# Kernel tuning notes

Hardware: AMD Instinct MI355X
Metric: run time of the kernel (lower is better)

## Reference

```python
import jax, jax.numpy as jnp
import numpy as np

DIM = 4096
N_HEADS = 32
HEAD_DIM = DIM // N_HEADS  # 128
BSZ = 2
SEQLEN = 2048


def setup_inputs() -> dict:
    key = jax.random.key(0)
    ks = jax.random.split(key, 8)
    x = jax.random.normal(ks[0], (BSZ, SEQLEN, DIM), dtype=jnp.float32)
    # rotary frequencies (LLaMA): theta = 10000^{-2i/d}, angle = pos * theta
    inv_freq = 1.0 / (10000.0 ** (np.arange(0, HEAD_DIM, 2, dtype=np.float32) / HEAD_DIM))
    angles = np.arange(SEQLEN, dtype=np.float32)[:, None] * inv_freq[None, :]  # [S, hd/2]
    freqs_cos = jnp.asarray(np.cos(angles))
    freqs_sin = jnp.asarray(np.sin(angles))
    # causal additive mask [1,1,S,S]
    neg = jnp.float32(-1e9)
    mask = jnp.where(jnp.tril(jnp.ones((SEQLEN, SEQLEN), dtype=bool)), 0.0, neg)[None, None]
    scale = 0.02
    wq = jax.random.normal(ks[1], (DIM, DIM), dtype=jnp.float32) * scale
    wk = jax.random.normal(ks[2], (DIM, DIM), dtype=jnp.float32) * scale
    wv = jax.random.normal(ks[3], (DIM, DIM), dtype=jnp.float32) * scale
    wo = jax.random.normal(ks[4], (DIM, DIM), dtype=jnp.float32) * scale
    return {"x": x, "start_pos": 0, "freqs_cos": freqs_cos, "freqs_sin": freqs_sin,
            "mask": mask, "wq": wq, "wk": wk, "wv": wv, "wo": wo}


def _apply_rotary(t, cos, sin):
    # t: [B,S,H,hd]; cos/sin: [S,hd/2] -> broadcast [1,S,1,hd/2]
    t = t.reshape(*t.shape[:-1], HEAD_DIM // 2, 2)
    t0, t1 = t[..., 0], t[..., 1]
    c = cos[None, :, None, :]
    s = sin[None, :, None, :]
    r0 = t0 * c - t1 * s
    r1 = t0 * s + t1 * c
    return jnp.stack([r0, r1], axis=-1).reshape(*t0.shape[:-1], HEAD_DIM)


def reference(x, start_pos, freqs_cos, freqs_sin, mask, wq, wk, wv, wo):
    bsz, seqlen, _ = x.shape
    # QKV projections (nn.Linear: y = x @ W.T; weights stored [out,in])
    xq = (x @ wq.T).reshape(bsz, seqlen, N_HEADS, HEAD_DIM)
    xk = (x @ wk.T).reshape(bsz, seqlen, N_HEADS, HEAD_DIM)
    xv = (x @ wv.T).reshape(bsz, seqlen, N_HEADS, HEAD_DIM)
    xq = _apply_rotary(xq, freqs_cos, freqs_sin)
    xk = _apply_rotary(xk, freqs_cos, freqs_sin)
    # [B,H,S,hd]
    q = xq.transpose(0, 2, 1, 3)
    k = xk.transpose(0, 2, 1, 3)
    v = xv.transpose(0, 2, 1, 3)
    scale = 1.0 / jnp.sqrt(jnp.float32(HEAD_DIM))
    scores = jnp.einsum('bhqd,bhkd->bhqk', q, k) * scale + mask
    probs = jax.nn.softmax(scores, axis=-1)
    out = jnp.einsum('bhqk,bhkd->bhqd', probs, v)  # [B,H,S,hd]
    out = out.transpose(0, 2, 1, 3).reshape(bsz, seqlen, DIM)
    return out @ wo.T
```

## Files before the change

kernel.cpp:

```cpp
#include <hip/hip_runtime.h>

typedef unsigned short ushort_t;
typedef unsigned int u32;
typedef short bf16x8 __attribute__((ext_vector_type(8)));
typedef float f32x4 __attribute__((ext_vector_type(4)));
typedef float f32x16 __attribute__((ext_vector_type(16)));
typedef u32 u32x4 __attribute__((ext_vector_type(4)));

__device__ __forceinline__ ushort_t f2bf(float f) {
  u32 u = __builtin_bit_cast(u32, f);
  u += 0x7FFFu + ((u >> 16) & 1u);
  return (ushort_t)(u >> 16);
}
__device__ __forceinline__ float bf2f(u32 bits16) {
  return __builtin_bit_cast(float, bits16 << 16);
}

__global__ __launch_bounds__(256)
void cvt_kernel(const float* __restrict__ in, ushort_t* __restrict__ out) {
  const int i = blockIdx.x * 256 + threadIdx.x;
  const float4 a = ((const float4*)in)[(size_t)i * 2];
  const float4 b = ((const float4*)in)[(size_t)i * 2 + 1];
  uint4 r;
  r.x = (u32)f2bf(a.x) | ((u32)f2bf(a.y) << 16);
  r.y = (u32)f2bf(a.z) | ((u32)f2bf(a.w) << 16);
  r.z = (u32)f2bf(b.x) | ((u32)f2bf(b.y) << 16);
  r.w = (u32)f2bf(b.z) | ((u32)f2bf(b.w) << 16);
  ((uint4*)out)[i] = r;
}

template <int F32OUT>
__global__ __launch_bounds__(512, 2)
void gemm256(const ushort_t* __restrict__ A, const ushort_t* __restrict__ B,
             void* __restrict__ C) {
  constexpr int KD = 4096, ND = 4096;
  __shared__ ushort_t sA[2][2][128 * 64];
  __shared__ ushort_t sB[2][2][128 * 64];
  const int tid = threadIdx.x;
  const int lane = tid & 63, wave = tid >> 6;
  const int lq = lane & 15, g = lane >> 4;
  const int wm = wave >> 2, wn = wave & 3;
  const int id = blockIdx.x;
  const int swz = (id & 7) * 32 + (id >> 3);
  const int bm = (swz >> 4) * 256;
  const int bn = (swz & 15) * 256;
  const int csw = ((lane & 7) ^ (lane >> 3)) * 8;
  const int srow = lane >> 3;

  f32x4 acc[8][4];
#pragma unroll
  for (int m = 0; m < 8; ++m)
#pragma unroll
    for (int n = 0; n < 4; ++n) acc[m][n] = (f32x4)0.f;

#define STG(sbuf, G, rowb, t_, s_, h_)                                               \
  {                                                                                  \
    _Pragma("unroll") for (int i_ = 0; i_ < 2; ++i_) {                               \
      const int r0_ = wave * 16 + i_ * 8;                                            \
      const int tc_ = (t_) > 63 ? 63 : (t_);                                         \
      const ushort_t* src_ =                                                         \
          (G) + (size_t)((rowb) + (h_) * 128 + r0_ + srow) * KD + tc_ * 64 + csw;    \
      __builtin_amdgcn_global_load_lds(                                              \
          (const __attribute__((address_space(1))) u32*)src_,                        \
          (__attribute__((address_space(3))) u32*)&sbuf[s_][h_][r0_ * 64 + lane * 8],\
          16, 0, 0);                                                                 \
    }                                                                                \
  }
#define RD_A(S_, H_, mf_, kk_)                                                        \
  (*(const bf16x8*)&sA[S_][H_][(wm * 64 + (mf_) * 16 + lq) * 64 +                     \
                               ((((kk_) * 4 + g) ^ (lq & 7)) * 8)])
#define RD_B(S_, H_, nf_, kk_)                                                        \
  (*(const bf16x8*)&sB[S_][H_][(wn * 32 + (nf_) * 16 + lq) * 64 +                     \
                               ((((kk_) * 4 + g) ^ (lq & 7)) * 8)])
#define MM2(MB, B0R, B1R)                                                             \
  _Pragma("unroll") for (int mf = 0; mf < 4; ++mf)                                    \
    _Pragma("unroll") for (int nf = 0; nf < 2; ++nf)                                  \
      _Pragma("unroll") for (int kk = 0; kk < 2; ++kk) {                              \
        acc[(MB) + mf][nf] = __builtin_amdgcn_mfma_f32_16x16x32_bf16(                 \
            af[mf][kk], B0R[nf][kk], acc[(MB) + mf][nf], 0, 0, 0);                    \
        acc[(MB) + mf][2 + nf] = __builtin_amdgcn_mfma_f32_16x16x32_bf16(             \
            af[mf][kk], B1R[nf][kk], acc[(MB) + mf][2 + nf], 0, 0, 0);                \
      }

  STG(sA, A, bm, 0, 0, 0); STG(sA, A, bm, 0, 0, 1);
  STG(sB, B, bn, 0, 0, 0); STG(sB, B, bn, 0, 0, 1);
  asm volatile("s_waitcnt vmcnt(0)" ::: "memory");
  __builtin_amdgcn_s_barrier();
  __builtin_amdgcn_sched_barrier(0);

  bf16x8 af[4][2], b0[2][2], b1[2][2];

#define TILE(S_, T_)                                                                  \
  STG(sA, A, bm, (T_) + 1, (S_) ^ 1, 0);                                              \
  STG(sA, A, bm, (T_) + 1, (S_) ^ 1, 1);                                              \
  STG(sB, B, bn, (T_) + 1, (S_) ^ 1, 0);                                              \
  STG(sB, B, bn, (T_) + 1, (S_) ^ 1, 1);                                              \
  _Pragma("unroll") for (int mf = 0; mf < 4; ++mf)                                    \
    _Pragma("unroll") for (int kk = 0; kk < 2; ++kk)                                  \
      af[mf][kk] = RD_A(S_, 0, mf, kk);                                               \
  _Pragma("unroll") for (int nf = 0; nf < 2; ++nf)                                    \
    _Pragma("unroll") for (int kk = 0; kk < 2; ++kk) {                                \
      b0[nf][kk] = RD_B(S_, 0, nf, kk);                                               \
      b1[nf][kk] = RD_B(S_, 1, nf, kk);                                               \
    }                                                                                 \
  __builtin_amdgcn_s_setprio(1);                                                      \
  MM2(0, b0, b1);                                                                     \
  __builtin_amdgcn_s_setprio(0);                                                      \
  _Pragma("unroll") for (int mf = 0; mf < 4; ++mf)                                    \
    _Pragma("unroll") for (int kk = 0; kk < 2; ++kk)                                  \
      af[mf][kk] = RD_A(S_, 1, mf, kk);                                               \
  __builtin_amdgcn_s_setprio(1);                                                      \
  MM2(4, b0, b1);                                                                     \
  __builtin_amdgcn_s_setprio(0);                                                      \
  asm volatile("s_waitcnt vmcnt(0)" ::: "memory");                                    \
  __builtin_amdgcn_s_barrier();                                                       \
  __builtin_amdgcn_sched_barrier(0);

  for (int t = 0; t < 64; t += 2) {
    TILE(0, t)
    TILE(1, t + 1)
  }
#undef TILE
#undef STG
#undef RD_A
#undef RD_B
#undef MM2

#pragma unroll
  for (int m = 0; m < 8; ++m) {
    const int grow = bm + (m >> 2) * 128 + wm * 64 + (m & 3) * 16 + g * 4;
#pragma unroll
    for (int r = 0; r < 4; ++r)
#pragma unroll
      for (int n = 0; n < 4; ++n) {
        const int gcol = bn + (n >> 1) * 128 + wn * 32 + (n & 1) * 16 + lq;
        if (F32OUT)
          ((float*)C)[(size_t)(grow + r) * ND + gcol] = acc[m][n][r];
        else
          ((ushort_t*)C)[(size_t)(grow + r) * ND + gcol] = f2bf(acc[m][n][r]);
      }
  }
}

__global__ __launch_bounds__(256)
void rope_kernel(ushort_t* __restrict__ Q, ushort_t* __restrict__ K,
                 const float* __restrict__ fcos, const float* __restrict__ fsin) {
  const int gid = blockIdx.x * 256 + threadIdx.x;
  ushort_t* T = blockIdx.y ? K : Q;
  const float scale = blockIdx.y ? 1.f : 0.08838834764831845f;
  const int j8 = gid & 15;
  const int h = (gid >> 4) & 31;
  const int s = (gid >> 9) & 2047;
  const int b = gid >> 20;
  const size_t off = (size_t)(b * 2048 + s) * 4096 + h * 128 + j8 * 8;
  uint4 v = *(const uint4*)(T + off);
  const float4 c4 = *(const float4*)(fcos + s * 64 + j8 * 4);
  const float4 s4 = *(const float4*)(fsin + s * 64 + j8 * 4);
  u32 w[4] = {v.x, v.y, v.z, v.w};
  const float cc[4] = {c4.x, c4.y, c4.z, c4.w};
  const float ss[4] = {s4.x, s4.y, s4.z, s4.w};
#pragma unroll
  for (int p = 0; p < 4; ++p) {
    const float t0 = bf2f(w[p] & 0xffffu);
    const float t1 = bf2f(w[p] >> 16);
    const float r0 = (t0 * cc[p] - t1 * ss[p]) * scale;
    const float r1 = (t0 * ss[p] + t1 * cc[p]) * scale;
    w[p] = (u32)f2bf(r0) | ((u32)f2bf(r1) << 16);
  }
  v.x = w[0]; v.y = w[1]; v.z = w[2]; v.w = w[3];
  *(uint4*)(T + off) = v;
}

__global__ __launch_bounds__(256, 2)
void attn_kernel(const ushort_t* __restrict__ Q, const ushort_t* __restrict__ K,
                 const ushort_t* __restrict__ Vt, ushort_t* __restrict__ O) {
  __shared__ ushort_t sK[2][32 * 128];
  __shared__ ushort_t sV[2][128 * 32];
  __shared__ float sScr[4][32];

  const int lane = threadIdx.x & 63, wave = threadIdx.x >> 6;
  const int lq = lane & 31, hi = lane >> 5;
  const int bp = blockIdx.x;
  const int bh = bp >> 3, j = bp & 7;
  const int h = bh & 31, b = bh >> 5;
  const ushort_t* Kb_ = K + (size_t)(b * 2048) * 4096 + h * 128;
  const ushort_t* Vb_ = Vt + (size_t)(h * 128) * 4096 + b * 2048;

#define STAGE(buf, kt_)                                                              \
  {                                                                                  \
    const int kb_ = (kt_) * 32;                                                      \
    _Pragma("unroll")                                                                \
    for (int i_ = 0; i_ < 2; ++i_) {                                                 \
      const int c_ = wave + i_ * 4;                                                  \
      const int krow = c_ * 4 + (lane >> 4);                                         \
      const int kcol = (lane & 15) ^ (krow & 7);                                     \
      const ushort_t* ksrc = Kb_ + (size_t)(kb_ + krow) * 4096 + kcol * 8;           \
      __builtin_amdgcn_global_load_lds(                                              \
          (const __attribute__((address_space(1))) u32*)ksrc,                        \
          (__attribute__((address_space(3))) u32*)&sK[buf][c_ * 512 + lane * 8],     \
          16, 0, 0);                                                                 \
      const int sst = c_ * 64 + lane;                                                \
      const int dv = sst >> 2;                                                       \
      const int gl = (sst & 3) ^ ((sst >> 3) & 3);                                   \
      const ushort_t* vsrc = Vb_ + (size_t)dv * 4096 + kb_ + gl * 8;                 \
      __builtin_amdgcn_global_load_lds(                                              \
          (const __attribute__((address_space(1))) u32*)vsrc,                        \
          (__attribute__((address_space(3))) u32*)&sV[buf][sst * 8], 16, 0, 0);      \
    }                                                                                \
  }

  for (int ph = 0; ph < 2; ++ph) {
    const int qj = ph ? (15 - j) : j;
    const int qbase = qj * 128 + wave * 32;
    const int ntw = qj * 4 + wave + 1;
    const int ntmax = qj * 4 + 4;

    bf16x8 aq[8];
    const ushort_t* qrow = Q + (size_t)(b * 2048 + qbase + lq) * 4096 + h * 128 + hi * 8;
#pragma unroll
    for (int kf = 0; kf < 8; ++kf) aq[kf] = *(const bf16x8*)(qrow + kf * 16);

    f32x16 o[4];
#pragma unroll
    for (int dt = 0; dt < 4; ++dt) o[dt] = (f32x16)0.f;
    float m_run = -1e30f, l_run = 0.f;

    int cur = 0;
    STAGE(0, 0);
    __syncthreads();

    for (int kt = 0; kt < ntmax; ++kt) {
      if (kt + 1 < ntmax) STAGE(cur ^ 1, kt + 1);
      if (kt < ntw) {
        const int kb = kt * 32;
        f32x16 st = (f32x16)0.f;
#pragma unroll
        for (int kf = 0; kf < 8; ++kf) {
          const bf16x8 kfrag =
              *(const bf16x8*)&sK[cur][lq * 128 + (((kf * 2 + hi) ^ (lq & 7)) * 8)];
          st = __builtin_amdgcn_mfma_f32_32x32x16_bf16(kfrag, aq[kf], st, 0, 0, 0);
        }
        if (kt == ntw - 1) {
          const int q = qbase + lq;
#pragma unroll
          for (int r = 0; r < 16; ++r) {
            const int key = kb + (r & 3) + 8 * (r >> 2) + 4 * hi;
            if (key > q) st[r] = -1e30f;
          }
        }
        float tm = st[0];
#pragma unroll
        for (int r = 1; r < 16; ++r) tm = fmaxf(tm, st[r]);
        tm = fmaxf(tm, __shfl_xor(tm, 32));
        if (!__all(tm <= m_run + 8.f)) {
          const float mnew = fmaxf(m_run, tm);
          const float corr = __expf(m_run - mnew);
          m_run = mnew;
          l_run *= corr;
          if (hi == 0) sScr[wave][lq] = corr;
          float fr[16];
#pragma unroll
          for (int r = 0; r < 16; ++r)
            fr[r] = sScr[wave][(r & 3) + 8 * (r >> 2) + 4 * hi];
#pragma unroll
          for (int dt = 0; dt < 4; ++dt)
#pragma unroll
            for (int r = 0; r < 16; ++r) o[dt][r] *= fr[r];
        }
        float rs = 0.f;
#pragma unroll
        for (int r = 0; r < 16; ++r) { st[r] = __expf(st[r] - m_run); rs += st[r]; }
        rs += __shfl_xor(rs, 32);
        l_run += rs;
        u32 A_, B_, C_, D_, E_, F_, G_, H_;
#define CVTPK(d_, l_, h_) \
  asm("v_cvt_pk_bf16_f32 %0, %1, %2" : "=v"(d_) : "v"(l_), "v"(h_))
        CVTPK(A_, st[0], st[1]);  CVTPK(B_, st[4], st[5]);
        CVTPK(C_, st[2], st[3]);  CVTPK(D_, st[6], st[7]);
        CVTPK(E_, st[8], st[9]);  CVTPK(F_, st[12], st[13]);
        CVTPK(G_, st[10], st[11]); CVTPK(H_, st[14], st[15]);
#undef CVTPK
        asm volatile("v_permlane32_swap_b32 %0, %1" : "+v"(A_), "+v"(B_));
        asm volatile("v_permlane32_swap_b32 %0, %1" : "+v"(C_), "+v"(D_));
        asm volatile("v_permlane32_swap_b32 %0, %1" : "+v"(E_), "+v"(F_));
        asm volatile("v_permlane32_swap_b32 %0, %1" : "+v"(G_), "+v"(H_));
        const bf16x8 pa0 = __builtin_bit_cast(bf16x8, (u32x4){A_, C_, B_, D_});
        const bf16x8 pa1 = __builtin_bit_cast(bf16x8, (u32x4){E_, G_, F_, H_});
#pragma unroll
        for (int dt = 0; dt < 4; ++dt) {
          const int d0 = dt * 32 + lq;
          const int s0 = 4 * d0 + ((hi + 0) ^ ((d0 >> 1) & 3));
          const int s1 = 4 * d0 + ((hi + 2) ^ ((d0 >> 1) & 3));
          const bf16x8 vf0 = *(const bf16x8*)&sV[cur][s0 * 8];
          const bf16x8 vf1 = *(const bf16x8*)&sV[cur][s1 * 8];
          o[dt] = __builtin_amdgcn_mfma_f32_32x32x16_bf16(pa0, vf0, o[dt], 0, 0, 0);
          o[dt] = __builtin_amdgcn_mfma_f32_32x32x16_bf16(pa1, vf1, o[dt], 0, 0, 0);
        }
      }
      __syncthreads();
      cur ^= 1;
    }

    if (hi == 0) sScr[wave][lq] = 1.f / l_run;
    __syncthreads();
    const size_t obase = (size_t)(b * 2048 + qbase) * 4096 + h * 128;
#pragma unroll
    for (int r = 0; r < 16; ++r) {
      const int qr = (r & 3) + 8 * (r >> 2) + 4 * hi;
      const float f = sScr[wave][qr];
#pragma unroll
      for (int dt = 0; dt < 4; ++dt)
        O[obase + (size_t)qr * 4096 + dt * 32 + lq] = f2bf(o[dt][r] * f);
    }
    __syncthreads();
  }
#undef STAGE
}

extern "C" void kernel_launch(void* const* d_in, const int* in_sizes, int n_in,
                              void* d_out, int out_size, void* d_ws, size_t ws_size,
                              hipStream_t stream) {
  const float* x = (const float*)d_in[0];
  const float* fcos = (const float*)d_in[2];
  const float* fsin = (const float*)d_in[3];
  const float* wq = (const float*)d_in[5];
  const float* wk = (const float*)d_in[6];
  const float* wv = (const float*)d_in[7];
  const float* wo = (const float*)d_in[8];
  float* out = (float*)d_out;
  char* ws = (char*)d_ws;
  const size_t MB32 = 33554432;
  ushort_t* xb = (ushort_t*)(ws);
  ushort_t* wb = (ushort_t*)(ws + MB32);
  ushort_t* Qb = (ushort_t*)(ws + 2 * MB32);
  ushort_t* Kb = (ushort_t*)(ws + 3 * MB32);
  ushort_t* Vt = (ushort_t*)(ws + 4 * MB32);
  ushort_t* Ob = xb;

  const dim3 cb(256);
  const dim3 cg(8192);
  const dim3 gb(512);
  const dim3 gg(256);

  hipLaunchKernelGGL(cvt_kernel, cg, cb, 0, stream, x, xb);
  hipLaunchKernelGGL(cvt_kernel, cg, cb, 0, stream, wq, wb);
  hipLaunchKernelGGL((gemm256<0>), gg, gb, 0, stream, xb, wb, (void*)Qb);
  hipLaunchKernelGGL(cvt_kernel, cg, cb, 0, stream, wk, wb);
  hipLaunchKernelGGL((gemm256<0>), gg, gb, 0, stream, xb, wb, (void*)Kb);
  hipLaunchKernelGGL(cvt_kernel, cg, cb, 0, stream, wv, wb);
  hipLaunchKernelGGL((gemm256<0>), gg, gb, 0, stream, wb, xb, (void*)Vt);
  hipLaunchKernelGGL(rope_kernel, dim3(8192, 2), cb, 0, stream, Qb, Kb, fcos, fsin);
  hipLaunchKernelGGL(attn_kernel, dim3(512), cb, 0, stream, Qb, Kb, Vt, Ob);
  hipLaunchKernelGGL(cvt_kernel, cg, cb, 0, stream, wo, wb);
  hipLaunchKernelGGL((gemm256<1>), gg, gb, 0, stream, Ob, wb, (void*)out);
}
```

Before: 684.1 us.

## Switch projection GEMM to 32x32x16 MFMA with per-wave 128x64 tiles

```diff
diff --git a/kernel.cpp b/kernel.cpp
--- a/kernel.cpp
+++ b/kernel.cpp
@@ -38,8 +38,10 @@
   __shared__ ushort_t sB[2][2][128 * 64];
   const int tid = threadIdx.x;
   const int lane = tid & 63, wave = tid >> 6;
-  const int lq = lane & 15, g = lane >> 4;
+  const int lq32 = lane & 31, hi = lane >> 5;
   const int wm = wave >> 2, wn = wave & 3;
+  const int bh = wn >> 1;
+  const int bro = (wn & 1) * 64;
   const int id = blockIdx.x;
   const int swz = (id & 7) * 32 + (id >> 3);
   const int bm = (swz >> 4) * 256;
@@ -47,11 +49,11 @@
   const int csw = ((lane & 7) ^ (lane >> 3)) * 8;
   const int srow = lane >> 3;
 
-  f32x4 acc[8][4];
-#pragma unroll
-  for (int m = 0; m < 8; ++m)
-#pragma unroll
-    for (int n = 0; n < 4; ++n) acc[m][n] = (f32x4)0.f;
+  f32x16 acc[4][2];
+#pragma unroll
+  for (int m = 0; m < 4; ++m)
+#pragma unroll
+    for (int n = 0; n < 2; ++n) acc[m][n] = (f32x16)0.f;
 
 #define STG(sbuf, G, rowb, t_, s_, h_)                                               \
   {                                                                                  \
@@ -66,21 +68,12 @@
           16, 0, 0);                                                                 \
     }                                                                                \
   }
-#define RD_A(S_, H_, mf_, kk_)                                                        \
-  (*(const bf16x8*)&sA[S_][H_][(wm * 64 + (mf_) * 16 + lq) * 64 +                     \
-                               ((((kk_) * 4 + g) ^ (lq & 7)) * 8)])
-#define RD_B(S_, H_, nf_, kk_)                                                        \
-  (*(const bf16x8*)&sB[S_][H_][(wn * 32 + (nf_) * 16 + lq) * 64 +                     \
-                               ((((kk_) * 4 + g) ^ (lq & 7)) * 8)])
-#define MM2(MB, B0R, B1R)                                                             \
-  _Pragma("unroll") for (int mf = 0; mf < 4; ++mf)                                    \
-    _Pragma("unroll") for (int nf = 0; nf < 2; ++nf)                                  \
-      _Pragma("unroll") for (int kk = 0; kk < 2; ++kk) {                              \
-        acc[(MB) + mf][nf] = __builtin_amdgcn_mfma_f32_16x16x32_bf16(                 \
-            af[mf][kk], B0R[nf][kk], acc[(MB) + mf][nf], 0, 0, 0);                    \
-        acc[(MB) + mf][2 + nf] = __builtin_amdgcn_mfma_f32_16x16x32_bf16(             \
-            af[mf][kk], B1R[nf][kk], acc[(MB) + mf][2 + nf], 0, 0, 0);                \
-      }
+#define RD_A(S_, mf_, ks_)                                                            \
+  (*(const bf16x8*)&sA[S_][wm][((mf_) * 32 + lq32) * 64 +                             \
+                               ((((ks_) * 2 + hi) ^ (lq32 & 7)) * 8)])
+#define RD_B(S_, nf_, ks_)                                                            \
+  (*(const bf16x8*)&sB[S_][bh][(bro + (nf_) * 32 + lq32) * 64 +                       \
+                               ((((ks_) * 2 + hi) ^ (lq32 & 7)) * 8)])
 
   STG(sA, A, bm, 0, 0, 0); STG(sA, A, bm, 0, 0, 1);
   STG(sB, B, bn, 0, 0, 0); STG(sB, B, bn, 0, 0, 1);
@@ -88,30 +81,30 @@
   __builtin_amdgcn_s_barrier();
   __builtin_amdgcn_sched_barrier(0);
 
-  bf16x8 af[4][2], b0[2][2], b1[2][2];
+  bf16x8 af[4][2], bf[2][2];
+
+#define CLUSTER(S_, C_)                                                               \
+  _Pragma("unroll") for (int mf = 0; mf < 4; ++mf)                                    \
+    _Pragma("unroll") for (int j = 0; j < 2; ++j)                                     \
+      af[mf][j] = RD_A(S_, mf, (C_) * 2 + j);                                         \
+  _Pragma("unroll") for (int nf = 0; nf < 2; ++nf)                                    \
+    _Pragma("unroll") for (int j = 0; j < 2; ++j)                                     \
+      bf[nf][j] = RD_B(S_, nf, (C_) * 2 + j);                                         \
+  __builtin_amdgcn_s_setprio(1);                                                      \
+  _Pragma("unroll") for (int mf = 0; mf < 4; ++mf)                                    \
+    _Pragma("unroll") for (int nf = 0; nf < 2; ++nf)                                  \
+      _Pragma("unroll") for (int j = 0; j < 2; ++j)                                   \
+        acc[mf][nf] = __builtin_amdgcn_mfma_f32_32x32x16_bf16(                        \
+            af[mf][j], bf[nf][j], acc[mf][nf], 0, 0, 0);                              \
+  __builtin_amdgcn_s_setprio(0);
 
 #define TILE(S_, T_)                                                                  \
   STG(sA, A, bm, (T_) + 1, (S_) ^ 1, 0);                                              \
   STG(sA, A, bm, (T_) + 1, (S_) ^ 1, 1);                                              \
+  CLUSTER(S_, 0)                                                                      \
   STG(sB, B, bn, (T_) + 1, (S_) ^ 1, 0);                                              \
   STG(sB, B, bn, (T_) + 1, (S_) ^ 1, 1);                                              \
-  _Pragma("unroll") for (int mf = 0; mf < 4; ++mf)                                    \
-    _Pragma("unroll") for (int kk = 0; kk < 2; ++kk)                                  \
-      af[mf][kk] = RD_A(S_, 0, mf, kk);                                               \
-  _Pragma("unroll") for (int nf = 0; nf < 2; ++nf)                                    \
-    _Pragma("unroll") for (int kk = 0; kk < 2; ++kk) {                                \
-      b0[nf][kk] = RD_B(S_, 0, nf, kk);                                               \
-      b1[nf][kk] = RD_B(S_, 1, nf, kk);                                               \
-    }                                                                                 \
-  __builtin_amdgcn_s_setprio(1);                                                      \
-  MM2(0, b0, b1);                                                                     \
-  __builtin_amdgcn_s_setprio(0);                                                      \
-  _Pragma("unroll") for (int mf = 0; mf < 4; ++mf)                                    \
-    _Pragma("unroll") for (int kk = 0; kk < 2; ++kk)                                  \
-      af[mf][kk] = RD_A(S_, 1, mf, kk);                                               \
-  __builtin_amdgcn_s_setprio(1);                                                      \
-  MM2(4, b0, b1);                                                                     \
-  __builtin_amdgcn_s_setprio(0);                                                      \
+  CLUSTER(S_, 1)                                                                      \
   asm volatile("s_waitcnt vmcnt(0)" ::: "memory");                                    \
   __builtin_amdgcn_s_barrier();                                                       \
   __builtin_amdgcn_sched_barrier(0);
@@ -121,25 +114,25 @@
     TILE(1, t + 1)
   }
 #undef TILE
+#undef CLUSTER
 #undef STG
 #undef RD_A
 #undef RD_B
-#undef MM2
-
-#pragma unroll
-  for (int m = 0; m < 8; ++m) {
-    const int grow = bm + (m >> 2) * 128 + wm * 64 + (m & 3) * 16 + g * 4;
-#pragma unroll
-    for (int r = 0; r < 4; ++r)
-#pragma unroll
-      for (int n = 0; n < 4; ++n) {
-        const int gcol = bn + (n >> 1) * 128 + wn * 32 + (n & 1) * 16 + lq;
+
+#pragma unroll
+  for (int mf = 0; mf < 4; ++mf)
+#pragma unroll
+    for (int nf = 0; nf < 2; ++nf) {
+      const int gcol = bn + wn * 64 + nf * 32 + lq32;
+#pragma unroll
+      for (int r = 0; r < 16; ++r) {
+        const int grow = bm + wm * 128 + mf * 32 + (r & 3) + 8 * (r >> 2) + 4 * hi;
         if (F32OUT)
-          ((float*)C)[(size_t)(grow + r) * ND + gcol] = acc[m][n][r];
+          ((float*)C)[(size_t)grow * ND + gcol] = acc[mf][nf][r];
         else
-          ((ushort_t*)C)[(size_t)(grow + r) * ND + gcol] = f2bf(acc[m][n][r]);
+          ((ushort_t*)C)[(size_t)grow * ND + gcol] = f2bf(acc[mf][nf][r]);
       }
-  }
+    }
 }
 
 __global__ __launch_bounds__(256)
```

Result: slower. 762.2 us (+11.4%).

## Fuse RoPE into Q/K GEMM epilogue and merge Q/K projections into one launch

Applied to the files above, without the earlier changes.

```diff
diff --git a/kernel.cpp b/kernel.cpp
--- a/kernel.cpp
+++ b/kernel.cpp
@@ -16,9 +16,8 @@
   return __builtin_bit_cast(float, bits16 << 16);
 }
 
-__global__ __launch_bounds__(256)
-void cvt_kernel(const float* __restrict__ in, ushort_t* __restrict__ out) {
-  const int i = blockIdx.x * 256 + threadIdx.x;
+__device__ __forceinline__ void cvt_body(const float* __restrict__ in,
+                                         ushort_t* __restrict__ out, int i) {
   const float4 a = ((const float4*)in)[(size_t)i * 2];
   const float4 b = ((const float4*)in)[(size_t)i * 2 + 1];
   uint4 r;
@@ -29,10 +28,27 @@
   ((uint4*)out)[i] = r;
 }
 
-template <int F32OUT>
+__global__ __launch_bounds__(256)
+void cvt_kernel(const float* __restrict__ in, ushort_t* __restrict__ out) {
+  cvt_body(in, out, blockIdx.x * 256 + threadIdx.x);
+}
+
+__global__ __launch_bounds__(256)
+void cvt3_kernel(const float* __restrict__ i0, ushort_t* __restrict__ o0,
+                 const float* __restrict__ i1, ushort_t* __restrict__ o1,
+                 const float* __restrict__ i2, ushort_t* __restrict__ o2) {
+  const int i = blockIdx.x * 256 + threadIdx.x;
+  const float* in = blockIdx.y == 0 ? i0 : (blockIdx.y == 1 ? i1 : i2);
+  ushort_t* out = blockIdx.y == 0 ? o0 : (blockIdx.y == 1 ? o1 : o2);
+  cvt_body(in, out, i);
+}
+
+template <int F32OUT, int ROPE>
 __global__ __launch_bounds__(512, 2)
-void gemm256(const ushort_t* __restrict__ A, const ushort_t* __restrict__ B,
-             void* __restrict__ C) {
+void gemm256(const ushort_t* __restrict__ A, const ushort_t* __restrict__ B0,
+             const ushort_t* __restrict__ B1, void* __restrict__ C0,
+             void* __restrict__ C1, const float* __restrict__ fcos,
+             const float* __restrict__ fsin) {
   constexpr int KD = 4096, ND = 4096;
   __shared__ ushort_t sA[2][2][128 * 64];
   __shared__ ushort_t sB[2][2][128 * 64];
@@ -41,9 +57,16 @@
   const int lq = lane & 15, g = lane >> 4;
   const int wm = wave >> 2, wn = wave & 3;
   const int id = blockIdx.x;
-  const int swz = (id & 7) * 32 + (id >> 3);
-  const int bm = (swz >> 4) * 256;
-  const int bn = (swz & 15) * 256;
+  int bm, bn;
+  if (ROPE) {
+    const int swz = (id & 7) * 64 + (id >> 3);
+    bm = (swz >> 5) * 256; bn = (swz & 31) * 256;
+  } else {
+    const int swz = (id & 7) * 32 + (id >> 3);
+    bm = (swz >> 4) * 256; bn = (swz & 15) * 256;
+  }
+  const ushort_t* Bt = (ROPE && bn >= 4096) ? B1 : B0;
+  const int bnl = ROPE ? (bn & 4095) : bn;
   const int csw = ((lane & 7) ^ (lane >> 3)) * 8;
   const int srow = lane >> 3;
 
@@ -66,12 +89,14 @@
           16, 0, 0);                                                                 \
     }                                                                                \
   }
+  const char* bA0 = (const char*)sA + (wm * 64 + lq) * 128 + ((g ^ (lq & 7)) * 16);
+  const char* bA1 = (const char*)sA + (wm * 64 + lq) * 128 + (((4 + g) ^ (lq & 7)) * 16);
+  const char* bB0p = (const char*)sB + (wn * 32 + lq) * 128 + ((g ^ (lq & 7)) * 16);
+  const char* bB1p = (const char*)sB + (wn * 32 + lq) * 128 + (((4 + g) ^ (lq & 7)) * 16);
 #define RD_A(S_, H_, mf_, kk_)                                                        \
-  (*(const bf16x8*)&sA[S_][H_][(wm * 64 + (mf_) * 16 + lq) * 64 +                     \
-                               ((((kk_) * 4 + g) ^ (lq & 7)) * 8)])
+  (*(const bf16x8*)(((kk_) ? bA1 : bA0) + (S_) * 32768 + (H_) * 16384 + (mf_) * 2048))
 #define RD_B(S_, H_, nf_, kk_)                                                        \
-  (*(const bf16x8*)&sB[S_][H_][(wn * 32 + (nf_) * 16 + lq) * 64 +                     \
-                               ((((kk_) * 4 + g) ^ (lq & 7)) * 8)])
+  (*(const bf16x8*)(((kk_) ? bB1p : bB0p) + (S_) * 32768 + (H_) * 16384 + (nf_) * 2048))
 #define MM2(MB, B0R, B1R)                                                             \
   _Pragma("unroll") for (int mf = 0; mf < 4; ++mf)                                    \
     _Pragma("unroll") for (int nf = 0; nf < 2; ++nf)                                  \
@@ -83,7 +108,7 @@
       }
 
   STG(sA, A, bm, 0, 0, 0); STG(sA, A, bm, 0, 0, 1);
-  STG(sB, B, bn, 0, 0, 0); STG(sB, B, bn, 0, 0, 1);
+  STG(sB, Bt, bnl, 0, 0, 0); STG(sB, Bt, bnl, 0, 0, 1);
   asm volatile("s_waitcnt vmcnt(0)" ::: "memory");
   __builtin_amdgcn_s_barrier();
   __builtin_amdgcn_sched_barrier(0);
@@ -93,8 +118,8 @@
 #define TILE(S_, T_)                                                                  \
   STG(sA, A, bm, (T_) + 1, (S_) ^ 1, 0);                                              \
   STG(sA, A, bm, (T_) + 1, (S_) ^ 1, 1);                                              \
-  STG(sB, B, bn, (T_) + 1, (S_) ^ 1, 0);                                              \
-  STG(sB, B, bn, (T_) + 1, (S_) ^ 1, 1);                                              \
+  STG(sB, Bt, bnl, (T_) + 1, (S_) ^ 1, 0);                                            \
+  STG(sB, Bt, bnl, (T_) + 1, (S_) ^ 1, 1);                                            \
   _Pragma("unroll") for (int mf = 0; mf < 4; ++mf)                                    \
     _Pragma("unroll") for (int kk = 0; kk < 2; ++kk)                                  \
       af[mf][kk] = RD_A(S_, 0, mf, kk);                                               \
@@ -126,49 +151,34 @@
 #undef RD_B
 #undef MM2
 
+  ushort_t* Ct = (ushort_t*)((ROPE && bn >= 4096) ? C1 : C0);
+  const float qsc = (ROPE && bn < 4096) ? 0.08838834764831845f : 1.f;
 #pragma unroll
   for (int m = 0; m < 8; ++m) {
     const int grow = bm + (m >> 2) * 128 + wm * 64 + (m & 3) * 16 + g * 4;
 #pragma unroll
-    for (int r = 0; r < 4; ++r)
+    for (int r = 0; r < 4; ++r) {
+      const int row = grow + r;
 #pragma unroll
       for (int n = 0; n < 4; ++n) {
-        const int gcol = bn + (n >> 1) * 128 + wn * 32 + (n & 1) * 16 + lq;
-        if (F32OUT)
-          ((float*)C)[(size_t)(grow + r) * ND + gcol] = acc[m][n][r];
-        else
-          ((ushort_t*)C)[(size_t)(grow + r) * ND + gcol] = f2bf(acc[m][n][r]);
+        const int gcol = bnl + (n >> 1) * 128 + wn * 32 + (n & 1) * 16 + lq;
+        if (ROPE) {
+          const int s = row & 2047;
+          const int p = (gcol >> 1) & 63;
+          const float cv = fcos[s * 64 + p];
+          const float sv = fsin[s * 64 + p];
+          const float self = acc[m][n][r];
+          const float other = __shfl_xor(self, 1);
+          const float sgn = (lq & 1) ? sv : -sv;
+          Ct[(size_t)row * ND + gcol] = f2bf((self * cv + other * sgn) * qsc);
+        } else if (F32OUT) {
+          ((float*)C0)[(size_t)row * ND + gcol] = acc[m][n][r];
+        } else {
+          ((ushort_t*)C0)[(size_t)row * ND + gcol] = f2bf(acc[m][n][r]);
+        }
       }
-  }
-}
-
-__global__ __launch_bounds__(256)
-void rope_kernel(ushort_t* __restrict__ Q, ushort_t* __restrict__ K,
-                 const float* __restrict__ fcos, const float* __restrict__ fsin) {
-  const int gid = blockIdx.x * 256 + threadIdx.x;
-  ushort_t* T = blockIdx.y ? K : Q;
-  const float scale = blockIdx.y ? 1.f : 0.08838834764831845f;
-  const int j8 = gid & 15;
-  const int h = (gid >> 4) & 31;
-  const int s = (gid >> 9) & 2047;
-  const int b = gid >> 20;
-  const size_t off = (size_t)(b * 2048 + s) * 4096 + h * 128 + j8 * 8;
-  uint4 v = *(const uint4*)(T + off);
-  const float4 c4 = *(const float4*)(fcos + s * 64 + j8 * 4);
-  const float4 s4 = *(const float4*)(fsin + s * 64 + j8 * 4);
-  u32 w[4] = {v.x, v.y, v.z, v.w};
-  const float cc[4] = {c4.x, c4.y, c4.z, c4.w};
-  const float ss[4] = {s4.x, s4.y, s4.z, s4.w};
-#pragma unroll
-  for (int p = 0; p < 4; ++p) {
-    const float t0 = bf2f(w[p] & 0xffffu);
-    const float t1 = bf2f(w[p] >> 16);
-    const float r0 = (t0 * cc[p] - t1 * ss[p]) * scale;
-    const float r1 = (t0 * ss[p] + t1 * cc[p]) * scale;
-    w[p] = (u32)f2bf(r0) | ((u32)f2bf(r1) << 16);
-  }
-  v.x = w[0]; v.y = w[1]; v.z = w[2]; v.w = w[3];
-  *(uint4*)(T + off) = v;
+    }
+  }
 }
 
 __global__ __launch_bounds__(256, 2)
@@ -340,17 +350,15 @@
   const dim3 cb(256);
   const dim3 cg(8192);
   const dim3 gb(512);
-  const dim3 gg(256);
-
-  hipLaunchKernelGGL(cvt_kernel, cg, cb, 0, stream, x, xb);
-  hipLaunchKernelGGL(cvt_kernel, cg, cb, 0, stream, wq, wb);
-  hipLaunchKernelGGL((gemm256<0>), gg, gb, 0, stream, xb, wb, (void*)Qb);
-  hipLaunchKernelGGL(cvt_kernel, cg, cb, 0, stream, wk, wb);
-  hipLaunchKernelGGL((gemm256<0>), gg, gb, 0, stream, xb, wb, (void*)Kb);
+
+  hipLaunchKernelGGL(cvt3_kernel, dim3(8192, 3), cb, 0, stream, x, xb, wq, wb, wk, Vt);
+  hipLaunchKernelGGL((gemm256<0, 1>), dim3(512), gb, 0, stream, xb, wb, Vt,
+                     (void*)Qb, (void*)Kb, fcos, fsin);
   hipLaunchKernelGGL(cvt_kernel, cg, cb, 0, stream, wv, wb);
-  hipLaunchKernelGGL((gemm256<0>), gg, gb, 0, stream, wb, xb, (void*)Vt);
-  hipLaunchKernelGGL(rope_kernel, dim3(8192, 2), cb, 0, stream, Qb, Kb, fcos, fsin);
+  hipLaunchKernelGGL((gemm256<0, 0>), dim3(256), gb, 0, stream, wb, xb, xb,
+                     (void*)Vt, (void*)Vt, fcos, fsin);
   hipLaunchKernelGGL(attn_kernel, dim3(512), cb, 0, stream, Qb, Kb, Vt, Ob);
   hipLaunchKernelGGL(cvt_kernel, cg, cb, 0, stream, wo, wb);
-  hipLaunchKernelGGL((gemm256<1>), gg, gb, 0, stream, Ob, wb, (void*)out);
-}
+  hipLaunchKernelGGL((gemm256<1, 0>), dim3(256), gb, 0, stream, Ob, wb, wb,
+                     (void*)out, (void*)out, fcos, fsin);
+}
```

After: 673.5 us. No clear change (-1.5%).
